# Performance work log

Hardware: AMD Instinct MI355X
Metric: run time of the kernel (lower is better)

## Reference

```python
import jax, jax.numpy as jnp
import numpy as np

N = 8192
E = 262144
NFEAT = 200
NHID = 128
NOUT = 16
CLUSTERS = (10, 5)


def _layernorm(x, g, b, eps=1e-5):
    mu = jnp.mean(x, axis=-1, keepdims=True)
    var = jnp.var(x, axis=-1, keepdims=True)
    return (x - mu) / jnp.sqrt(var + eps) * g + b


def _gumbel_softmax_hard(logits, g, tau=1.0):
    # straight-through gumbel softmax (hard=True), dim=1
    y = jax.nn.softmax((logits + g) / tau, axis=1)
    hard = jax.nn.one_hot(jnp.argmax(y, axis=1), y.shape[1], dtype=y.dtype)
    return hard + y - jax.lax.stop_gradient(y)


def _row_normalize(x, eps=1e-12):
    n = jnp.linalg.norm(x, axis=1, keepdims=True)
    return x / jnp.maximum(n, eps)


def setup_inputs() -> dict:
    key = jax.random.key(0)
    ks = jax.random.split(key, 20)
    u0 = jax.random.uniform(ks[3], (N, CLUSTERS[0]), minval=1e-6, maxval=1.0 - 1e-6)
    u1 = jax.random.uniform(ks[4], (CLUSTERS[0], CLUSTERS[1]), minval=1e-6, maxval=1.0 - 1e-6)
    s = 0.05
    return {
        'x': jax.random.normal(ks[0], (N, NFEAT), dtype=jnp.float32),
        'edge_index': jax.random.randint(ks[1], (2, E), 0, N, dtype=jnp.int32),
        'edge_weight': jax.random.uniform(ks[2], (E,), dtype=jnp.float32),
        'gumbel0': -jnp.log(-jnp.log(u0)),
        'gumbel1': -jnp.log(-jnp.log(u1)),
        # GCN params (2 layers, layernorm)
        'Wg1': jax.random.normal(ks[5], (NHID, NFEAT)) * s,
        'bg1': jnp.zeros((NHID,)),
        'ln1_g': jnp.ones((NHID,)), 'ln1_b': jnp.zeros((NHID,)),
        'Wg2': jax.random.normal(ks[6], (NHID, NHID)) * s,
        'bg2': jnp.zeros((NHID,)),
        'ln2_g': jnp.ones((NHID,)), 'ln2_b': jnp.zeros((NHID,)),
        # per-level pool + encoder linears
        'pool0_W': jax.random.normal(ks[7], (CLUSTERS[0], NHID)) * s,
        'pool0_b': jnp.zeros((CLUSTERS[0],)),
        'pool1_W': jax.random.normal(ks[8], (CLUSTERS[1], NHID)) * s,
        'pool1_b': jnp.zeros((CLUSTERS[1],)),
        'enc0_W': jax.random.normal(ks[9], (NHID, NHID)) * s,
        'enc0_b': jnp.zeros((NHID,)),
        'enc1_W': jax.random.normal(ks[10], (NHID, NHID)) * s,
        'enc1_b': jnp.zeros((NHID,)),
        'fc_W': jax.random.normal(ks[11], (NOUT, 3 * NHID)) * s,
        'fc_b': jnp.zeros((NOUT,)),
    }


def reference(x, edge_index, edge_weight, gumbel0, gumbel1,
              Wg1, bg1, ln1_g, ln1_b, Wg2, bg2, ln2_g, ln2_b,
              pool0_W, pool0_b, pool1_W, pool1_b,
              enc0_W, enc0_b, enc1_W, enc1_b, fc_W, fc_b):
    src, dst = edge_index[0], edge_index[1]

    def agg(h):  # weighted neighbor sum: out[i] = sum_{e: dst_e=i} w_e * h[src_e]
        return jax.ops.segment_sum(h[src] * edge_weight[:, None], dst, num_segments=N)

    # bottom GCN encoder (2 layers, layernorm)
    h = agg(x) @ Wg1.T + bg1
    h = jax.nn.relu(_layernorm(h, ln1_g, ln1_b))
    h = agg(h) @ Wg2.T + bg2
    h = _layernorm(h, ln2_g, ln2_b)
    latent = jax.nn.relu(h)  # [N, nhid]
    all_latents = [latent]

    # dense adjacency (to_dense_adj)
    adj = jnp.zeros((N, N), dtype=x.dtype).at[src, dst].add(edge_weight)

    pools = [(pool0_W, pool0_b), (pool1_W, pool1_b)]
    encs = [(enc0_W, enc0_b), (enc1_W, enc1_b)]
    gumbels = [gumbel0, gumbel1]
    product = None
    for level in range(len(CLUSTERS)):
        pW, pb = pools[level]
        eW, eb = encs[level]
        assign = _gumbel_softmax_hard(latent @ pW.T + pb, gumbels[level])  # [n_l, K]
        product = assign if level == 0 else product @ assign  # [N, K]
        xc = _row_normalize(assign.T @ latent)  # [K, nhid]
        adj = assign.T @ adj @ assign  # [K, K]
        adj = adj / jnp.sum(adj + 1e-8)
        latent = jax.nn.relu((adj @ xc) @ eW.T + eb)  # [K, nhid]
        all_latents.append(product @ latent)  # [N, nhid]

    rep = jnp.concatenate(all_latents, axis=1)  # [N, 3*nhid]
    return rep @ fc_W.T + fc_b
```

## Files before the change

kernel.cpp:

```cpp
#include <hip/hip_runtime.h>

#define N_NODES 8192
#define N_EDGES 262144
#define NFEAT 200
#define NHID 128

template<int K>
__global__ __launch_bounds__(128) void gemm_rows(const float* __restrict__ A,
                                                 const float* __restrict__ W,
                                                 float* __restrict__ C,
                                                 int nrows) {
    __shared__ float a_s[8 * K];
    int row0 = blockIdx.x * 8;
    const float* Ab = A + (size_t)row0 * K;
    for (int idx = threadIdx.x; idx < 8 * K; idx += 128) a_s[idx] = Ab[idx];
    __syncthreads();
    int j = threadIdx.x;
    float acc[8] = {0.f, 0.f, 0.f, 0.f, 0.f, 0.f, 0.f, 0.f};
    const float4* W4 = (const float4*)(W + (size_t)j * K);
    for (int k4 = 0; k4 < K / 4; ++k4) {
        float4 w = W4[k4];
        int k = k4 * 4;
        #pragma unroll
        for (int r = 0; r < 8; ++r) {
            const float* ar = a_s + r * K + k;
            acc[r] += ar[0] * w.x + ar[1] * w.y + ar[2] * w.z + ar[3] * w.w;
        }
    }
    #pragma unroll
    for (int r = 0; r < 8; ++r) C[(size_t)(row0 + r) * 128 + j] = acc[r];
}

__global__ __launch_bounds__(256) void hist_kernel(const int* __restrict__ ei,
                                                   int* __restrict__ deg, int E) {
    const int* dst = ei + E;
    for (int e = blockIdx.x * blockDim.x + threadIdx.x; e < E; e += gridDim.x * blockDim.x)
        atomicAdd(&deg[dst[e]], 1);
}

__global__ __launch_bounds__(256) void scan_kernel(const int* __restrict__ deg,
                                                   int* __restrict__ row_start,
                                                   int* __restrict__ cursor) {
    __shared__ int part[256];
    __shared__ int partx[257];
    int tid = threadIdx.x;
    int base = tid * 32;
    int s = 0;
    for (int i = 0; i < 32; ++i) s += deg[base + i];
    part[tid] = s;
    __syncthreads();
    if (tid == 0) {
        int run = 0;
        for (int i = 0; i < 256; ++i) { partx[i] = run; run += part[i]; }
        partx[256] = run;
    }
    __syncthreads();
    int run = partx[tid];
    for (int i = 0; i < 32; ++i) {
        row_start[base + i] = run;
        cursor[base + i] = run;
        run += deg[base + i];
    }
    if (tid == 255) row_start[N_NODES] = run;
}

__global__ __launch_bounds__(256) void scatter_kernel(const int* __restrict__ ei,
                                                      const float* __restrict__ ew,
                                                      int* __restrict__ cursor,
                                                      int* __restrict__ ssort,
                                                      float* __restrict__ wsort, int E) {
    int e = blockIdx.x * blockDim.x + threadIdx.x;
    if (e < E) {
        int d = ei[E + e];
        int pos = atomicAdd(&cursor[d], 1);
        ssort[pos] = ei[e];
        wsort[pos] = ew[e];
    }
}

__global__ __launch_bounds__(256) void agg_ln_csr(const int* __restrict__ row_start,
                                                  const int* __restrict__ ssort,
                                                  const float* __restrict__ wsort,
                                                  const float* __restrict__ H,
                                                  float* __restrict__ out,
                                                  const float* __restrict__ bias,
                                                  const float* __restrict__ g,
                                                  const float* __restrict__ b) {
    int wave = (blockIdx.x * blockDim.x + threadIdx.x) >> 6;
    int lane = threadIdx.x & 63;
    int s0 = row_start[wave], s1 = row_start[wave + 1];
    float ax0 = 0.f, ay0 = 0.f, ax1 = 0.f, ay1 = 0.f;
    int e = s0;
    for (; e + 1 < s1; e += 2) {
        int sA = ssort[e], sB = ssort[e + 1];
        float wA = wsort[e], wB = wsort[e + 1];
        float2 vA = *(const float2*)(H + (size_t)sA * 128 + lane * 2);
        float2 vB = *(const float2*)(H + (size_t)sB * 128 + lane * 2);
        ax0 += wA * vA.x; ay0 += wA * vA.y;
        ax1 += wB * vB.x; ay1 += wB * vB.y;
    }
    if (e < s1) {
        int sA = ssort[e];
        float wA = wsort[e];
        float2 vA = *(const float2*)(H + (size_t)sA * 128 + lane * 2);
        ax0 += wA * vA.x; ay0 += wA * vA.y;
    }
    float2 bs = *(const float2*)(bias + lane * 2);
    float vx = ax0 + ax1 + bs.x;
    float vy = ay0 + ay1 + bs.y;
    float s = vx + vy;
    float ss = vx * vx + vy * vy;
    for (int off = 32; off; off >>= 1) {
        s += __shfl_xor(s, off, 64);
        ss += __shfl_xor(ss, off, 64);
    }
    float mu = s * (1.f / 128.f);
    float var = ss * (1.f / 128.f) - mu * mu;
    float rs = rsqrtf(var + 1e-5f);
    float2 gg = *(const float2*)(g + lane * 2);
    float2 bb = *(const float2*)(b + lane * 2);
    float y0 = fmaxf((vx - mu) * rs * gg.x + bb.x, 0.f);
    float y1 = fmaxf((vy - mu) * rs * gg.y + bb.y, 0.f);
    *(float2*)(out + (size_t)wave * 128 + lane * 2) = make_float2(y0, y1);
}

__global__ __launch_bounds__(256) void pool0_kernel(const float* __restrict__ latent,
                                                    const float* __restrict__ pW,
                                                    const float* __restrict__ pb,
                                                    const float* __restrict__ gum,
                                                    int* __restrict__ c0) {
    __shared__ float Ws[10 * 128];
    __shared__ float bs[10];
    for (int i = threadIdx.x; i < 1280; i += 256) Ws[i] = pW[i];
    if (threadIdx.x < 10) bs[threadIdx.x] = pb[threadIdx.x];
    __syncthreads();
    int lane = threadIdx.x & 63;
    int sub = lane & 7;
    int row = (blockIdx.x * 4 + (threadIdx.x >> 6)) * 8 + (lane >> 3);

    const float4* lp = (const float4*)(latent + (size_t)row * 128 + sub * 16);
    float4 x0 = lp[0], x1 = lp[1], x2 = lp[2], x3 = lp[3];
    float2 gj[5];
    #pragma unroll
    for (int j = 0; j < 5; ++j) gj[j] = *(const float2*)(gum + (size_t)row * 10 + j * 2);

    float p[10];
    #pragma unroll
    for (int k = 0; k < 10; ++k) {
        const float4* wk = (const float4*)(Ws + k * 128 + sub * 16);
        float4 w0 = wk[0], w1 = wk[1], w2 = wk[2], w3 = wk[3];
        float a = x0.x * w0.x + x0.y * w0.y + x0.z * w0.z + x0.w * w0.w;
        a += x1.x * w1.x + x1.y * w1.y + x1.z * w1.z + x1.w * w1.w;
        a += x2.x * w2.x + x2.y * w2.y + x2.z * w2.z + x2.w * w2.w;
        a += x3.x * w3.x + x3.y * w3.y + x3.z * w3.z + x3.w * w3.w;
        p[k] = a;
    }
    #pragma unroll
    for (int off = 1; off < 8; off <<= 1) {
        #pragma unroll
        for (int k = 0; k < 10; ++k) p[k] += __shfl_xor(p[k], off, 64);
    }
    int best = 0;
    float bv = p[0] + bs[0] + gj[0].x;
    #pragma unroll
    for (int k = 1; k < 10; ++k) {
        float gk = (k & 1) ? gj[k >> 1].y : gj[k >> 1].x;
        float z = p[k] + bs[k] + gk;
        if (z > bv) { bv = z; best = k; }
    }
    if (sub == 0) c0[row] = best;
}

__global__ __launch_bounds__(256) void xc0_partial(const float* __restrict__ latent,
                                                   const int* __restrict__ c0,
                                                   float* __restrict__ partials) {
    __shared__ float acc[1280];
    for (int i = threadIdx.x; i < 1280; i += 256) acc[i] = 0.f;
    __syncthreads();
    int d = threadIdx.x & 127;
    int half = threadIdx.x >> 7;
    int base = blockIdx.x * 32;
    #pragma unroll
    for (int it = 0; it < 16; ++it) {
        int row = base + it * 2 + half;
        int c = c0[row];
        float v = latent[(size_t)row * 128 + d];
        atomicAdd(&acc[c * 128 + d], v);
    }
    __syncthreads();
    for (int i = threadIdx.x; i < 1280; i += 256)
        partials[(size_t)blockIdx.x * 1280 + i] = acc[i];
}

__global__ __launch_bounds__(256) void xc0_reduce(const float* __restrict__ partials,
                                                  float* __restrict__ xc0) {
    int k = blockIdx.x;
    int d = threadIdx.x & 127;
    int half = threadIdx.x >> 7;
    int b0 = half * 128;
    float s0 = 0.f, s1 = 0.f, s2 = 0.f, s3 = 0.f;
    for (int b = b0; b < b0 + 128; b += 4) {
        s0 += partials[(size_t)(b    ) * 1280 + k * 128 + d];
        s1 += partials[(size_t)(b + 1) * 1280 + k * 128 + d];
        s2 += partials[(size_t)(b + 2) * 1280 + k * 128 + d];
        s3 += partials[(size_t)(b + 3) * 1280 + k * 128 + d];
    }
    __shared__ float sm[256];
    sm[threadIdx.x] = (s0 + s1) + (s2 + s3);
    __syncthreads();
    if (threadIdx.x < 128) xc0[k * 128 + d] = sm[threadIdx.x] + sm[threadIdx.x + 128];
}

__global__ __launch_bounds__(256) void adj_pool_kernel(const int* __restrict__ ei,
                                                       const float* __restrict__ ew,
                                                       const int* __restrict__ c0,
                                                       float* __restrict__ A0, int E) {
    __shared__ float As[100];
    for (int i = threadIdx.x; i < 100; i += 256) As[i] = 0.f;
    __syncthreads();
    const int* src = ei;
    const int* dst = ei + E;
    for (int e = blockIdx.x * blockDim.x + threadIdx.x; e < E; e += gridDim.x * blockDim.x) {
        int a = c0[src[e]], b = c0[dst[e]];
        atomicAdd(&As[a * 10 + b], ew[e]);
    }
    __syncthreads();
    for (int i = threadIdx.x; i < 100; i += 256) atomicAdd(&A0[i], As[i]);
}

__global__ __launch_bounds__(256) void small_kernel(const float* __restrict__ xc0,
                                                    const float* __restrict__ A0,
                                                    const float* __restrict__ gum1,
                                                    const float* __restrict__ p1W,
                                                    const float* __restrict__ p1b,
                                                    const float* __restrict__ e0W,
                                                    const float* __restrict__ e0b,
                                                    const float* __restrict__ e1W,
                                                    const float* __restrict__ e1b,
                                                    const float* __restrict__ fcW,
                                                    const float* __restrict__ fcb,
                                                    float* __restrict__ tbl) {
    __shared__ float xc0n[10 * 128];
    __shared__ float adj0[100];
    __shared__ float m0[10 * 128];
    __shared__ float l1[10 * 128];
    __shared__ float xc1n[5 * 128];
    __shared__ float l2[5 * 128];
    __shared__ float A1[25];
    __shared__ int c1[10];
    __shared__ float red[4];

    int tid = threadIdx.x;
    int wid = tid >> 6, lane = tid & 63;

    for (int r = wid; r < 10; r += 4) {
        float2 v = *(const float2*)(xc0 + r * 128 + lane * 2);
        float ss = v.x * v.x + v.y * v.y;
        for (int off = 32; off; off >>= 1) ss += __shfl_xor(ss, off, 64);
        float sc = 1.f / fmaxf(sqrtf(ss), 1e-12f);
        xc0n[r * 128 + lane * 2] = v.x * sc;
        xc0n[r * 128 + lane * 2 + 1] = v.y * sc;
    }
    __syncthreads();
    if (tid == 0) {
        float s = 0.f;
        for (int i = 0; i < 100; ++i) s += A0[i];
        red[0] = s + 1e-6f;
    }
    __syncthreads();
    if (tid < 100) adj0[tid] = A0[tid] / red[0];
    __syncthreads();
    for (int idx = tid; idx < 1280; idx += 256) {
        int r = idx >> 7, d = idx & 127;
        float acc = 0.f;
        #pragma unroll
        for (int a = 0; a < 10; ++a) acc += adj0[r * 10 + a] * xc0n[a * 128 + d];
        m0[idx] = acc;
    }
    __syncthreads();
    for (int idx = tid; idx < 1280; idx += 256) {
        int r = idx >> 7, d = idx & 127;
        float acc = e0b[d];
        const float* wrow = e0W + d * 128;
        for (int k = 0; k < 128; ++k) acc += m0[r * 128 + k] * wrow[k];
        l1[idx] = fmaxf(acc, 0.f);
    }
    __syncthreads();
    if (tid < 10) {
        int best = 0;
        float bv = -1e30f;
        for (int j = 0; j < 5; ++j) {
            float acc = p1b[j] + gum1[tid * 5 + j];
            const float* wrow = p1W + j * 128;
            for (int k = 0; k < 128; ++k) acc += l1[tid * 128 + k] * wrow[k];
            if (acc > bv) { bv = acc; best = j; }
        }
        c1[tid] = best;
    }
    __syncthreads();
    for (int idx = tid; idx < 640; idx += 256) {
        int m = idx >> 7, d = idx & 127;
        float acc = 0.f;
        #pragma unroll
        for (int k = 0; k < 10; ++k)
            if (c1[k] == m) acc += l1[k * 128 + d];
        xc1n[idx] = acc;
    }
    __syncthreads();
    for (int r = wid; r < 5; r += 4) {
        float2 v = *(const float2*)(xc1n + r * 128 + lane * 2);
        float ss = v.x * v.x + v.y * v.y;
        for (int off = 32; off; off >>= 1) ss += __shfl_xor(ss, off, 64);
        float sc = 1.f / fmaxf(sqrtf(ss), 1e-12f);
        xc1n[r * 128 + lane * 2] = v.x * sc;
        xc1n[r * 128 + lane * 2 + 1] = v.y * sc;
    }
    __syncthreads();
    if (tid < 25) {
        int m = tid / 5, n = tid % 5;
        float acc = 0.f;
        for (int a = 0; a < 10; ++a)
            for (int b = 0; b < 10; ++b)
                if (c1[a] == m && c1[b] == n) acc += adj0[a * 10 + b];
        A1[tid] = acc;
    }
    __syncthreads();
    if (tid == 0) {
        float s = 0.f;
        for (int i = 0; i < 25; ++i) s += A1[i];
        red[1] = s + 25e-8f;
    }
    __syncthreads();
    float den1 = red[1];
    for (int idx = tid; idx < 640; idx += 256) {
        int r = idx >> 7, d = idx & 127;
        float acc = 0.f;
        #pragma unroll
        for (int a = 0; a < 5; ++a) acc += A1[r * 5 + a] * xc1n[a * 128 + d];
        m0[idx] = acc / den1;
    }
    __syncthreads();
    for (int idx = tid; idx < 640; idx += 256) {
        int r = idx >> 7, d = idx & 127;
        float acc = e1b[d];
        const float* wrow = e1W + d * 128;
        for (int k = 0; k < 128; ++k) acc += m0[r * 128 + k] * wrow[k];
        l2[idx] = fmaxf(acc, 0.f);
    }
    __syncthreads();
    for (int idx = tid; idx < 160; idx += 256) {
        int k = idx >> 4, o = idx & 15;
        float acc = fcb[o];
        const float* fB = fcW + o * 384 + 128;
        const float* fC = fcW + o * 384 + 256;
        const float* a1 = l1 + k * 128;
        const float* a2 = l2 + c1[k] * 128;
        for (int d = 0; d < 128; ++d) acc += a1[d] * fB[d] + a2[d] * fC[d];
        tbl[idx] = acc;
    }
}

__global__ __launch_bounds__(256) void out_kernel(const float* __restrict__ latent,
                                                  const int* __restrict__ c0,
                                                  const float* __restrict__ tbl,
                                                  const float* __restrict__ fcW,
                                                  float* __restrict__ out, int nrows) {
    __shared__ float fA[16 * 128];
    __shared__ float ts[160];
    for (int i = threadIdx.x; i < 2048; i += 256) {
        int o = i >> 7, d = i & 127;
        fA[i] = fcW[o * 384 + d];
    }
    for (int i = threadIdx.x; i < 160; i += 256) ts[i] = tbl[i];
    __syncthreads();
    int wid = threadIdx.x >> 6, lane = threadIdx.x & 63;
    int row = blockIdx.x * 4 + wid;
    if (row >= nrows) return;
    float2 x = *(const float2*)(latent + (size_t)row * 128 + lane * 2);
    float p[16];
    #pragma unroll
    for (int o = 0; o < 16; ++o)
        p[o] = x.x * fA[o * 128 + lane * 2] + x.y * fA[o * 128 + lane * 2 + 1];
    for (int off = 32; off; off >>= 1) {
        #pragma unroll
        for (int o = 0; o < 16; ++o) p[o] += __shfl_xor(p[o], off, 64);
    }
    if (lane < 16) {
        int c = c0[row];
        out[(size_t)row * 16 + lane] = p[lane] + ts[c * 16 + lane];
    }
}

extern "C" void kernel_launch(void* const* d_in, const int* in_sizes, int n_in,
                              void* d_out, int out_size, void* d_ws, size_t ws_size,
                              hipStream_t stream) {
    const float* x    = (const float*)d_in[0];
    const int*   ei   = (const int*)d_in[1];
    const float* ew   = (const float*)d_in[2];
    const float* g0   = (const float*)d_in[3];
    const float* g1   = (const float*)d_in[4];
    const float* Wg1  = (const float*)d_in[5];
    const float* bg1  = (const float*)d_in[6];
    const float* ln1g = (const float*)d_in[7];
    const float* ln1b = (const float*)d_in[8];
    const float* Wg2  = (const float*)d_in[9];
    const float* bg2  = (const float*)d_in[10];
    const float* ln2g = (const float*)d_in[11];
    const float* ln2b = (const float*)d_in[12];
    const float* p0W  = (const float*)d_in[13];
    const float* p0b  = (const float*)d_in[14];
    const float* p1W  = (const float*)d_in[15];
    const float* p1b  = (const float*)d_in[16];
    const float* e0W  = (const float*)d_in[17];
    const float* e0b  = (const float*)d_in[18];
    const float* e1W  = (const float*)d_in[19];
    const float* e1b  = (const float*)d_in[20];
    const float* fcW  = (const float*)d_in[21];
    const float* fcb  = (const float*)d_in[22];
    float* out = (float*)d_out;

    float* ws   = (float*)d_ws;
    float* bufA = ws;
    float* bufB = bufA + (size_t)N_NODES * 128;
    int*   c0   = (int*)(bufB + (size_t)N_NODES * 128);
    float* xc0  = (float*)(c0 + N_NODES);
    float* A0   = xc0 + 1280;
    float* tbl  = A0 + 100;
    int*   deg  = (int*)(tbl + 160);
    int*   row_start = deg + N_NODES;
    int*   cursor    = row_start + N_NODES + 1;
    int*   ssort     = cursor + N_NODES;
    float* wsort     = (float*)(ssort + N_EDGES);
    float* partials  = bufA;

    hipMemsetAsync(deg, 0, N_NODES * sizeof(int), stream);
    hist_kernel<<<256, 256, 0, stream>>>(ei, deg, N_EDGES);
    scan_kernel<<<1, 256, 0, stream>>>(deg, row_start, cursor);
    scatter_kernel<<<N_EDGES / 256, 256, 0, stream>>>(ei, ew, cursor, ssort, wsort, N_EDGES);

    gemm_rows<NFEAT><<<N_NODES / 8, 128, 0, stream>>>(x, Wg1, bufA, N_NODES);
    agg_ln_csr<<<N_NODES / 4, 256, 0, stream>>>(row_start, ssort, wsort, bufA, bufB,
                                                bg1, ln1g, ln1b);

    gemm_rows<NHID><<<N_NODES / 8, 128, 0, stream>>>(bufB, Wg2, bufA, N_NODES);
    agg_ln_csr<<<N_NODES / 4, 256, 0, stream>>>(row_start, ssort, wsort, bufA, bufB,
                                                bg2, ln2g, ln2b);

    pool0_kernel<<<256, 256, 0, stream>>>(bufB, p0W, p0b, g0, c0);
    xc0_partial<<<256, 256, 0, stream>>>(bufB, c0, partials);
    xc0_reduce<<<10, 256, 0, stream>>>(partials, xc0);
    hipMemsetAsync(A0, 0, 100 * sizeof(float), stream);
    adj_pool_kernel<<<256, 256, 0, stream>>>(ei, ew, c0, A0, N_EDGES);

    small_kernel<<<1, 256, 0, stream>>>(xc0, A0, g1, p1W, p1b, e0W, e0b, e1W, e1b,
                                        fcW, fcb, tbl);

    out_kernel<<<N_NODES / 4, 256, 0, stream>>>(bufB, c0, tbl, fcW, out, N_NODES);
}
```

Before: 211.6 us.

## Fuse launches, pack CSR edges as int2, widen aggregation unroll and output kernel

Several kernel launches are merged: the degree histogram rides along with the first GEMM as extra blocks, the pool assignment and per-cluster feature partial sums happen in one kernel, and the adjacency pooling shares a launch with the partial reduction. The two memsets are merged into one. CSR edges are stored as packed (src, weight) int2 pairs so each edge needs one load, and the aggregation loop is unrolled to four independent gathers. The output projection now processes eight rows per wave with float4 loads instead of one row per wave. Together these aim to cut launch overhead and memory latency, at the cost of more shared-memory atomics and more complex kernels.

```diff
diff --git a/kernel.cpp b/kernel.cpp
--- a/kernel.cpp
+++ b/kernel.cpp
@@ -6,12 +6,11 @@
 #define NHID 128
 
 template<int K>
-__global__ __launch_bounds__(128) void gemm_rows(const float* __restrict__ A,
-                                                 const float* __restrict__ W,
-                                                 float* __restrict__ C,
-                                                 int nrows) {
+__device__ __forceinline__ void gemm_body(const float* __restrict__ A,
+                                          const float* __restrict__ W,
+                                          float* __restrict__ C, int bid) {
     __shared__ float a_s[8 * K];
-    int row0 = blockIdx.x * 8;
+    int row0 = bid * 8;
     const float* Ab = A + (size_t)row0 * K;
     for (int idx = threadIdx.x; idx < 8 * K; idx += 128) a_s[idx] = Ab[idx];
     __syncthreads();
@@ -31,11 +30,25 @@
     for (int r = 0; r < 8; ++r) C[(size_t)(row0 + r) * 128 + j] = acc[r];
 }
 
-__global__ __launch_bounds__(256) void hist_kernel(const int* __restrict__ ei,
-                                                   int* __restrict__ deg, int E) {
-    const int* dst = ei + E;
-    for (int e = blockIdx.x * blockDim.x + threadIdx.x; e < E; e += gridDim.x * blockDim.x)
-        atomicAdd(&deg[dst[e]], 1);
+template<int K>
+__global__ __launch_bounds__(128) void gemm_rows(const float* __restrict__ A,
+                                                 const float* __restrict__ W,
+                                                 float* __restrict__ C) {
+    gemm_body<K>(A, W, C, blockIdx.x);
+}
+
+__global__ __launch_bounds__(128) void gemm1_hist(const float* __restrict__ A,
+                                                  const float* __restrict__ W,
+                                                  float* __restrict__ C,
+                                                  const int* __restrict__ ei,
+                                                  int* __restrict__ deg) {
+    if (blockIdx.x < N_NODES / 8) {
+        gemm_body<NFEAT>(A, W, C, blockIdx.x);
+    } else {
+        const int* dst = ei + N_EDGES;
+        for (int e = (blockIdx.x - N_NODES / 8) * 128 + threadIdx.x; e < N_EDGES; e += 64 * 128)
+            atomicAdd(&deg[dst[e]], 1);
+    }
 }
 
 __global__ __launch_bounds__(256) void scan_kernel(const int* __restrict__ deg,
@@ -67,20 +80,17 @@
 __global__ __launch_bounds__(256) void scatter_kernel(const int* __restrict__ ei,
                                                       const float* __restrict__ ew,
                                                       int* __restrict__ cursor,
-                                                      int* __restrict__ ssort,
-                                                      float* __restrict__ wsort, int E) {
+                                                      int2* __restrict__ esort, int E) {
     int e = blockIdx.x * blockDim.x + threadIdx.x;
     if (e < E) {
         int d = ei[E + e];
         int pos = atomicAdd(&cursor[d], 1);
-        ssort[pos] = ei[e];
-        wsort[pos] = ew[e];
+        esort[pos] = make_int2(ei[e], __float_as_int(ew[e]));
     }
 }
 
 __global__ __launch_bounds__(256) void agg_ln_csr(const int* __restrict__ row_start,
-                                                  const int* __restrict__ ssort,
-                                                  const float* __restrict__ wsort,
+                                                  const int2* __restrict__ esort,
                                                   const float* __restrict__ H,
                                                   float* __restrict__ out,
                                                   const float* __restrict__ bias,
@@ -90,24 +100,30 @@
     int lane = threadIdx.x & 63;
     int s0 = row_start[wave], s1 = row_start[wave + 1];
     float ax0 = 0.f, ay0 = 0.f, ax1 = 0.f, ay1 = 0.f;
+    float ax2 = 0.f, ay2 = 0.f, ax3 = 0.f, ay3 = 0.f;
     int e = s0;
-    for (; e + 1 < s1; e += 2) {
-        int sA = ssort[e], sB = ssort[e + 1];
-        float wA = wsort[e], wB = wsort[e + 1];
-        float2 vA = *(const float2*)(H + (size_t)sA * 128 + lane * 2);
-        float2 vB = *(const float2*)(H + (size_t)sB * 128 + lane * 2);
-        ax0 += wA * vA.x; ay0 += wA * vA.y;
-        ax1 += wB * vB.x; ay1 += wB * vB.y;
-    }
-    if (e < s1) {
-        int sA = ssort[e];
-        float wA = wsort[e];
-        float2 vA = *(const float2*)(H + (size_t)sA * 128 + lane * 2);
-        ax0 += wA * vA.x; ay0 += wA * vA.y;
+    for (; e + 3 < s1; e += 4) {
+        int2 p0 = esort[e], p1 = esort[e + 1], p2 = esort[e + 2], p3 = esort[e + 3];
+        float2 v0 = *(const float2*)(H + (size_t)p0.x * 128 + lane * 2);
+        float2 v1 = *(const float2*)(H + (size_t)p1.x * 128 + lane * 2);
+        float2 v2 = *(const float2*)(H + (size_t)p2.x * 128 + lane * 2);
+        float2 v3 = *(const float2*)(H + (size_t)p3.x * 128 + lane * 2);
+        float w0 = __int_as_float(p0.y), w1 = __int_as_float(p1.y);
+        float w2 = __int_as_float(p2.y), w3 = __int_as_float(p3.y);
+        ax0 += w0 * v0.x; ay0 += w0 * v0.y;
+        ax1 += w1 * v1.x; ay1 += w1 * v1.y;
+        ax2 += w2 * v2.x; ay2 += w2 * v2.y;
+        ax3 += w3 * v3.x; ay3 += w3 * v3.y;
+    }
+    for (; e < s1; ++e) {
+        int2 p0 = esort[e];
+        float2 v0 = *(const float2*)(H + (size_t)p0.x * 128 + lane * 2);
+        float w0 = __int_as_float(p0.y);
+        ax0 += w0 * v0.x; ay0 += w0 * v0.y;
     }
     float2 bs = *(const float2*)(bias + lane * 2);
-    float vx = ax0 + ax1 + bs.x;
-    float vy = ay0 + ay1 + bs.y;
+    float vx = (ax0 + ax1) + (ax2 + ax3) + bs.x;
+    float vy = (ay0 + ay1) + (ay2 + ay3) + bs.y;
     float s = vx + vy;
     float ss = vx * vx + vy * vy;
     for (int off = 32; off; off >>= 1) {
@@ -124,19 +140,21 @@
     *(float2*)(out + (size_t)wave * 128 + lane * 2) = make_float2(y0, y1);
 }
 
-__global__ __launch_bounds__(256) void pool0_kernel(const float* __restrict__ latent,
-                                                    const float* __restrict__ pW,
-                                                    const float* __restrict__ pb,
-                                                    const float* __restrict__ gum,
-                                                    int* __restrict__ c0) {
+__global__ __launch_bounds__(256) void pool0_xc0(const float* __restrict__ latent,
+                                                 const float* __restrict__ pW,
+                                                 const float* __restrict__ pb,
+                                                 const float* __restrict__ gum,
+                                                 int* __restrict__ c0,
+                                                 float* __restrict__ partials) {
     __shared__ float Ws[10 * 128];
     __shared__ float bs[10];
-    for (int i = threadIdx.x; i < 1280; i += 256) Ws[i] = pW[i];
+    __shared__ float acc[1280];
+    for (int i = threadIdx.x; i < 1280; i += 256) { Ws[i] = pW[i]; acc[i] = 0.f; }
     if (threadIdx.x < 10) bs[threadIdx.x] = pb[threadIdx.x];
     __syncthreads();
     int lane = threadIdx.x & 63;
     int sub = lane & 7;
-    int row = (blockIdx.x * 4 + (threadIdx.x >> 6)) * 8 + (lane >> 3);
+    int row = blockIdx.x * 32 + (threadIdx.x >> 6) * 8 + (lane >> 3);
 
     const float4* lp = (const float4*)(latent + (size_t)row * 128 + sub * 16);
     float4 x0 = lp[0], x1 = lp[1], x2 = lp[2], x3 = lp[3];
@@ -169,63 +187,55 @@
         if (z > bv) { bv = z; best = k; }
     }
     if (sub == 0) c0[row] = best;
-}
-
-__global__ __launch_bounds__(256) void xc0_partial(const float* __restrict__ latent,
-                                                   const int* __restrict__ c0,
-                                                   float* __restrict__ partials) {
-    __shared__ float acc[1280];
-    for (int i = threadIdx.x; i < 1280; i += 256) acc[i] = 0.f;
-    __syncthreads();
-    int d = threadIdx.x & 127;
-    int half = threadIdx.x >> 7;
-    int base = blockIdx.x * 32;
-    #pragma unroll
-    for (int it = 0; it < 16; ++it) {
-        int row = base + it * 2 + half;
-        int c = c0[row];
-        float v = latent[(size_t)row * 128 + d];
-        atomicAdd(&acc[c * 128 + d], v);
-    }
+    float* ap = acc + best * 128 + sub * 16;
+    atomicAdd(ap + 0, x0.x);  atomicAdd(ap + 1, x0.y);
+    atomicAdd(ap + 2, x0.z);  atomicAdd(ap + 3, x0.w);
+    atomicAdd(ap + 4, x1.x);  atomicAdd(ap + 5, x1.y);
+    atomicAdd(ap + 6, x1.z);  atomicAdd(ap + 7, x1.w);
+    atomicAdd(ap + 8, x2.x);  atomicAdd(ap + 9, x2.y);
+    atomicAdd(ap + 10, x2.z); atomicAdd(ap + 11, x2.w);
+    atomicAdd(ap + 12, x3.x); atomicAdd(ap + 13, x3.y);
+    atomicAdd(ap + 14, x3.z); atomicAdd(ap + 15, x3.w);
     __syncthreads();
     for (int i = threadIdx.x; i < 1280; i += 256)
         partials[(size_t)blockIdx.x * 1280 + i] = acc[i];
 }
 
-__global__ __launch_bounds__(256) void xc0_reduce(const float* __restrict__ partials,
-                                                  float* __restrict__ xc0) {
-    int k = blockIdx.x;
-    int d = threadIdx.x & 127;
-    int half = threadIdx.x >> 7;
-    int b0 = half * 128;
-    float s0 = 0.f, s1 = 0.f, s2 = 0.f, s3 = 0.f;
-    for (int b = b0; b < b0 + 128; b += 4) {
-        s0 += partials[(size_t)(b    ) * 1280 + k * 128 + d];
-        s1 += partials[(size_t)(b + 1) * 1280 + k * 128 + d];
-        s2 += partials[(size_t)(b + 2) * 1280 + k * 128 + d];
-        s3 += partials[(size_t)(b + 3) * 1280 + k * 128 + d];
-    }
-    __shared__ float sm[256];
-    sm[threadIdx.x] = (s0 + s1) + (s2 + s3);
-    __syncthreads();
-    if (threadIdx.x < 128) xc0[k * 128 + d] = sm[threadIdx.x] + sm[threadIdx.x + 128];
-}
-
-__global__ __launch_bounds__(256) void adj_pool_kernel(const int* __restrict__ ei,
-                                                       const float* __restrict__ ew,
-                                                       const int* __restrict__ c0,
-                                                       float* __restrict__ A0, int E) {
-    __shared__ float As[100];
-    for (int i = threadIdx.x; i < 100; i += 256) As[i] = 0.f;
-    __syncthreads();
-    const int* src = ei;
-    const int* dst = ei + E;
-    for (int e = blockIdx.x * blockDim.x + threadIdx.x; e < E; e += gridDim.x * blockDim.x) {
-        int a = c0[src[e]], b = c0[dst[e]];
-        atomicAdd(&As[a * 10 + b], ew[e]);
-    }
-    __syncthreads();
-    for (int i = threadIdx.x; i < 100; i += 256) atomicAdd(&A0[i], As[i]);
+__global__ __launch_bounds__(256) void adj_xc0(const int* __restrict__ ei,
+                                               const float* __restrict__ ew,
+                                               const int* __restrict__ c0,
+                                               float* __restrict__ A0,
+                                               const float* __restrict__ partials,
+                                               float* __restrict__ xc0, int E) {
+    if (blockIdx.x < 256) {
+        __shared__ float As[100];
+        for (int i = threadIdx.x; i < 100; i += 256) As[i] = 0.f;
+        __syncthreads();
+        const int* src = ei;
+        const int* dst = ei + E;
+        for (int e = blockIdx.x * 256 + threadIdx.x; e < E; e += 256 * 256) {
+            int a = c0[src[e]], b = c0[dst[e]];
+            atomicAdd(&As[a * 10 + b], ew[e]);
+        }
+        __syncthreads();
+        for (int i = threadIdx.x; i < 100; i += 256) atomicAdd(&A0[i], As[i]);
+    } else {
+        int k = blockIdx.x - 256;
+        int d = threadIdx.x & 127;
+        int half = threadIdx.x >> 7;
+        int b0 = half * 128;
+        float s0 = 0.f, s1 = 0.f, s2 = 0.f, s3 = 0.f;
+        for (int b = b0; b < b0 + 128; b += 4) {
+            s0 += partials[(size_t)(b    ) * 1280 + k * 128 + d];
+            s1 += partials[(size_t)(b + 1) * 1280 + k * 128 + d];
+            s2 += partials[(size_t)(b + 2) * 1280 + k * 128 + d];
+            s3 += partials[(size_t)(b + 3) * 1280 + k * 128 + d];
+        }
+        __shared__ float sm[256];
+        sm[threadIdx.x] = (s0 + s1) + (s2 + s3);
+        __syncthreads();
+        if (threadIdx.x < 128) xc0[k * 128 + d] = sm[threadIdx.x] + sm[threadIdx.x + 128];
+    }
 }
 
 __global__ __launch_bounds__(256) void small_kernel(const float* __restrict__ xc0,
@@ -364,7 +374,7 @@
                                                   const int* __restrict__ c0,
                                                   const float* __restrict__ tbl,
                                                   const float* __restrict__ fcW,
-                                                  float* __restrict__ out, int nrows) {
+                                                  float* __restrict__ out) {
     __shared__ float fA[16 * 128];
     __shared__ float ts[160];
     for (int i = threadIdx.x; i < 2048; i += 256) {
@@ -373,22 +383,31 @@
     }
     for (int i = threadIdx.x; i < 160; i += 256) ts[i] = tbl[i];
     __syncthreads();
-    int wid = threadIdx.x >> 6, lane = threadIdx.x & 63;
-    int row = blockIdx.x * 4 + wid;
-    if (row >= nrows) return;
-    float2 x = *(const float2*)(latent + (size_t)row * 128 + lane * 2);
+    int lane = threadIdx.x & 63;
+    int sub = lane & 7;
+    int row = blockIdx.x * 32 + (threadIdx.x >> 6) * 8 + (lane >> 3);
+    const float4* lp = (const float4*)(latent + (size_t)row * 128 + sub * 16);
+    float4 x0 = lp[0], x1 = lp[1], x2 = lp[2], x3 = lp[3];
     float p[16];
     #pragma unroll
-    for (int o = 0; o < 16; ++o)
-        p[o] = x.x * fA[o * 128 + lane * 2] + x.y * fA[o * 128 + lane * 2 + 1];
-    for (int off = 32; off; off >>= 1) {
+    for (int o = 0; o < 16; ++o) {
+        const float4* fo = (const float4*)(fA + o * 128 + sub * 16);
+        float4 w0 = fo[0], w1 = fo[1], w2 = fo[2], w3 = fo[3];
+        float a = x0.x * w0.x + x0.y * w0.y + x0.z * w0.z + x0.w * w0.w;
+        a += x1.x * w1.x + x1.y * w1.y + x1.z * w1.z + x1.w * w1.w;
+        a += x2.x * w2.x + x2.y * w2.y + x2.z * w2.z + x2.w * w2.w;
+        a += x3.x * w3.x + x3.y * w3.y + x3.z * w3.z + x3.w * w3.w;
+        p[o] = a;
+    }
+    #pragma unroll
+    for (int off = 1; off < 8; off <<= 1) {
         #pragma unroll
         for (int o = 0; o < 16; ++o) p[o] += __shfl_xor(p[o], off, 64);
     }
-    if (lane < 16) {
-        int c = c0[row];
-        out[(size_t)row * 16 + lane] = p[lane] + ts[c * 16 + lane];
-    }
+    int c = c0[row];
+    float2 r = make_float2(p[2 * sub] + ts[c * 16 + 2 * sub],
+                           p[2 * sub + 1] + ts[c * 16 + 2 * sub + 1]);
+    *(float2*)(out + (size_t)row * 16 + 2 * sub) = r;
 }
 
 extern "C" void kernel_launch(void* const* d_in, const int* in_sizes, int n_in,
@@ -424,36 +443,31 @@
     float* bufB = bufA + (size_t)N_NODES * 128;
     int*   c0   = (int*)(bufB + (size_t)N_NODES * 128);
     float* xc0  = (float*)(c0 + N_NODES);
-    float* A0   = xc0 + 1280;
-    float* tbl  = A0 + 100;
+    float* tbl  = xc0 + 1280;
     int*   deg  = (int*)(tbl + 160);
-    int*   row_start = deg + N_NODES;
-    int*   cursor    = row_start + N_NODES + 1;
-    int*   ssort     = cursor + N_NODES;
-    float* wsort     = (float*)(ssort + N_EDGES);
+    float* A0   = (float*)(deg + N_NODES);
+    int*   row_start = (int*)(A0 + 100);
+    int*   cursor    = row_start + N_NODES + 2;
+    int2*  esort     = (int2*)(cursor + N_NODES);
     float* partials  = bufA;
 
-    hipMemsetAsync(deg, 0, N_NODES * sizeof(int), stream);
-    hist_kernel<<<256, 256, 0, stream>>>(ei, deg, N_EDGES);
+    hipMemsetAsync(deg, 0, (N_NODES + 100) * sizeof(int), stream);
+
+    gemm1_hist<<<N_NODES / 8 + 64, 128, 0, stream>>>(x, Wg1, bufA, ei, deg);
     scan_kernel<<<1, 256, 0, stream>>>(deg, row_start, cursor);
-    scatter_kernel<<<N_EDGES / 256, 256, 0, stream>>>(ei, ew, cursor, ssort, wsort, N_EDGES);
-
-    gemm_rows<NFEAT><<<N_NODES / 8, 128, 0, stream>>>(x, Wg1, bufA, N_NODES);
-    agg_ln_csr<<<N_NODES / 4, 256, 0, stream>>>(row_start, ssort, wsort, bufA, bufB,
+    scatter_kernel<<<N_EDGES / 256, 256, 0, stream>>>(ei, ew, cursor, esort, N_EDGES);
+    agg_ln_csr<<<N_NODES / 4, 256, 0, stream>>>(row_start, esort, bufA, bufB,
                                                 bg1, ln1g, ln1b);
 
-    gemm_rows<NHID><<<N_NODES / 8, 128, 0, stream>>>(bufB, Wg2, bufA, N_NODES);
-    agg_ln_csr<<<N_NODES / 4, 256, 0, stream>>>(row_start, ssort, wsort, bufA, bufB,
+    gemm_rows<NHID><<<N_NODES / 8, 128, 0, stream>>>(bufB, Wg2, bufA);
+    agg_ln_csr<<<N_NODES / 4, 256, 0, stream>>>(row_start, esort, bufA, bufB,
                                                 bg2, ln2g, ln2b);
 
-    pool0_kernel<<<256, 256, 0, stream>>>(bufB, p0W, p0b, g0, c0);
-    xc0_partial<<<256, 256, 0, stream>>>(bufB, c0, partials);
-    xc0_reduce<<<10, 256, 0, stream>>>(partials, xc0);
-    hipMemsetAsync(A0, 0, 100 * sizeof(float), stream);
-    adj_pool_kernel<<<256, 256, 0, stream>>>(ei, ew, c0, A0, N_EDGES);
+    pool0_xc0<<<256, 256, 0, stream>>>(bufB, p0W, p0b, g0, c0, partials);
+    adj_xc0<<<266, 256, 0, stream>>>(ei, ew, c0, A0, partials, xc0, N_EDGES);
 
     small_kernel<<<1, 256, 0, stream>>>(xc0, A0, g1, p1W, p1b, e0W, e0b, e1W, e1b,
                                         fcW, fcb, tbl);
 
-    out_kernel<<<N_NODES / 4, 256, 0, stream>>>(bufB, c0, tbl, fcW, out, N_NODES);
-}
+    out_kernel<<<256, 256, 0, stream>>>(bufB, c0, tbl, fcW, out);
+}
```

New measurement: 181.3 us. 14.3% less time.
